# Performance work log

Hardware: AMD Instinct MI355X
Metric: run time of the kernel (lower is better)

The kernel has to match this reference:

```python
import jax, jax.numpy as jnp
import numpy as np

NUM_CLASSES = 2
THRESHOLD = 0.35
NEGPOS_RATIO = 7
VARIANCES = (0.1, 0.2)
B, P, O = 64, 16800, 64  # batch, num_priors, num_objs per image


def point_form(pr):
    # cxcywh -> xyxy
    return jnp.concatenate([pr[:, :2] - pr[:, 2:] / 2, pr[:, :2] + pr[:, 2:] / 2], axis=1)


def jaccard(a, b):
    # a: [A,4] xyxy, b: [Bx,4] xyxy -> IoU [A,Bx]
    lt = jnp.maximum(a[:, None, :2], b[None, :, :2])
    rb = jnp.minimum(a[:, None, 2:], b[None, :, 2:])
    wh = jnp.clip(rb - lt, 0.0)
    inter = wh[..., 0] * wh[..., 1]
    area_a = ((a[:, 2] - a[:, 0]) * (a[:, 3] - a[:, 1]))[:, None]
    area_b = ((b[:, 2] - b[:, 0]) * (b[:, 3] - b[:, 1]))[None, :]
    return inter / (area_a + area_b - inter)


def encode(matched, priors):
    # matched xyxy [P,4], priors cxcywh [P,4]
    g_cxcy = (matched[:, :2] + matched[:, 2:]) / 2 - priors[:, :2]
    g_cxcy = g_cxcy / (VARIANCES[0] * priors[:, 2:])
    g_wh = (matched[:, 2:] - matched[:, :2]) / priors[:, 2:]
    g_wh = jnp.log(g_wh) / VARIANCES[1]
    return jnp.concatenate([g_cxcy, g_wh], axis=1)


def encode_landm(matched, priors):
    # matched [P,10] -> [P,5,2]
    m = matched.reshape(-1, 5, 2)
    g = (m - priors[:, None, :2]) / (VARIANCES[0] * priors[:, None, 2:])
    return g.reshape(-1, 10)


def match_one(truths, labels, landms, priors):
    # truths [O,4], labels [O], landms [O,10]
    overlaps = jaccard(truths, point_form(priors))  # [O,P]
    best_prior_overlap = overlaps.max(axis=1)       # per-gt best IoU
    best_prior_idx = overlaps.argmax(axis=1)
    valid_gt = best_prior_overlap >= 0.2
    best_truth_overlap = overlaps.max(axis=0)       # per-prior best IoU
    best_truth_idx = overlaps.argmax(axis=0)
    # index_fill(2) only for valid gts (best_prior_idx_filter)
    bto = best_truth_overlap.at[best_prior_idx].set(
        jnp.where(valid_gt, 2.0, best_truth_overlap[best_prior_idx]))
    # ensure every gt keeps its best prior
    bti = best_truth_idx.at[best_prior_idx].set(jnp.arange(truths.shape[0]))
    matches = truths[bti]                  # [P,4]
    conf = labels[bti]                     # [P]
    conf = jnp.where(bto < THRESHOLD, 0.0, conf)
    loc = encode(matches, priors)
    landm = encode_landm(landms[bti], priors)
    return loc, conf, landm


def smooth_l1_sum(x, mask):
    ax = jnp.abs(x)
    v = jnp.where(ax < 1.0, 0.5 * ax * ax, ax - 0.5)
    return (v * mask).sum()


def setup_inputs() -> dict:
    key = jax.random.key(0)
    k1, k2, k3, k4, k5, k6, k7, k8 = jax.random.split(key, 8)
    loc_data = jax.random.normal(k1, (B, P, 4), jnp.float32)
    conf_data = jax.random.normal(k2, (B, P, NUM_CLASSES), jnp.float32)
    landm_data = jax.random.normal(k3, (B, P, 10), jnp.float32)
    # priors: cx,cy in (0,1), w,h in (0.02,0.22)
    cxy = jax.random.uniform(k4, (P, 2), jnp.float32)
    wh = jax.random.uniform(k5, (P, 2), jnp.float32) * 0.2 + 0.02
    priors = jnp.concatenate([cxy, wh], axis=1)
    # targets: valid corner boxes + landmarks + label in {1,-1}
    xy1 = jax.random.uniform(k6, (B, O, 2), jnp.float32) * 0.6
    bwh = jax.random.uniform(k7, (B, O, 2), jnp.float32) * 0.3 + 0.05
    boxes = jnp.concatenate([xy1, xy1 + bwh], axis=-1)
    lms = jax.random.uniform(k8, (B, O, 10), jnp.float32)
    lab = jnp.where(jax.random.uniform(jax.random.fold_in(key, 9), (B, O, 1)) < 0.3, -1.0, 1.0)
    targets = jnp.concatenate([boxes, lms, lab], axis=-1)
    return {"loc_data": loc_data, "conf_data": conf_data, "landm_data": landm_data,
            "priors": priors, "targets": targets}


def reference(loc_data, conf_data, landm_data, priors, targets):
    num = loc_data.shape[0]
    num_priors = priors.shape[0]
    truths = targets[:, :, :4]
    landms = targets[:, :, 4:14]
    labels = targets[:, :, -1]
    loc_t, conf_t, landm_t = jax.vmap(match_one, in_axes=(0, 0, 0, None))(
        truths, labels, landms, priors)  # [B,P,4], [B,P], [B,P,10]

    # landmark loss over conf_t > 0
    pos1 = conf_t > 0
    num_pos_landm = pos1.astype(jnp.int32).sum(axis=1, keepdims=True)
    N1 = jnp.maximum(num_pos_landm.sum().astype(jnp.float32), 1.0)
    loss_landm = smooth_l1_sum(landm_data - landm_t, pos1[..., None].astype(landm_data.dtype))

    # localization loss over conf_t != 0 ; conf_t[pos] = 1
    pos = conf_t != 0
    conf_t01 = jnp.where(pos, 1, 0)  # int {0,1}
    loss_l = smooth_l1_sum(loc_data - loc_t, pos[..., None].astype(loc_data.dtype))

    # hard negative mining on per-prior CE loss (global-max log_sum_exp, as in source)
    batch_conf = conf_data.reshape(-1, NUM_CLASSES)
    x_max = batch_conf.max()
    lse = jnp.log(jnp.exp(batch_conf - x_max).sum(axis=1, keepdims=True)) + x_max
    gathered = jnp.take_along_axis(batch_conf, conf_t01.reshape(-1, 1), axis=1)
    loss_c = (lse - gathered).reshape(num, -1)  # [B,P]; positives NOT zeroed (as in source)
    loss_idx = jnp.argsort(-loss_c, axis=1)
    idx_rank = jnp.argsort(loss_idx, axis=1)
    num_pos = pos.astype(jnp.int32).sum(axis=1, keepdims=True)  # [B,1]
    num_neg = jnp.minimum(NEGPOS_RATIO * num_pos, num_priors - 1)
    neg = idx_rank < num_neg  # [B,P]
    neg_pos = pos | neg

    # cross-entropy (sum) over selected pos+neg priors
    logp = jax.nn.log_softmax(conf_data, axis=-1)  # [B,P,C]
    ce = -jnp.take_along_axis(logp, conf_t01[..., None], axis=-1)[..., 0]
    loss_c_final = (ce * neg_pos.astype(ce.dtype)).sum()

    N = jnp.maximum(num_pos.sum().astype(jnp.float32), 1.0)
    return (loss_l / N, loss_c_final / N, loss_landm / N1)
```

## Files before the change

kernel.cpp:

```cpp
#include <hip/hip_runtime.h>
#include <math.h>

#define BN 64
#define PN 16800
#define ON 64
#define THRESH 0.35f
#define NEGPOS 7
#define GX 66
#define NBLK (BN * GX)
#define NBP 1024
#define NBTT (BN * GX)
#define NCELL 256
#define NBINS 4096
#define MAXM 4096
#define TAILT 104

struct GAcc {
  unsigned ticket;
  float sl, slm, sc;
  int np, np1;
  unsigned pad0, pad1;
};

__device__ __forceinline__ unsigned f2key(float f) {
  unsigned u = __float_as_uint(f);
  return (u & 0x80000000u) ? ~u : (u | 0x80000000u);
}
__device__ __forceinline__ float key2f(unsigned k) {
  unsigned u = (k & 0x80000000u) ? (k & 0x7FFFFFFFu) : ~k;
  return __uint_as_float(u);
}
__device__ __forceinline__ float sl1(float d) {
  float a = fabsf(d);
  return (a < 1.f) ? 0.5f * a * a : a - 0.5f;
}

__global__ void __launch_bounds__(1024) k_sort(const float* __restrict__ priors,
                                               float4* __restrict__ sbox,
                                               int* __restrict__ sorig,
                                               int* __restrict__ scell,
                                               int* __restrict__ inv,
                                               int* __restrict__ cellOff,
                                               unsigned* __restrict__ gmax,
                                               GAcc* __restrict__ gacc) {
  __shared__ unsigned cnt[NCELL];
  __shared__ unsigned cur[NCELL];
  __shared__ unsigned tmp[NCELL];
  int tid = threadIdx.x;
  if (tid < NCELL) cnt[tid] = 0;
  if (tid == 0) { gmax[0] = 0u; gmax[1] = 0u; }
  if (tid < 8) ((unsigned*)gacc)[tid] = 0;
  __syncthreads();
  float mw = 0.f, mh = 0.f;
  for (int p = tid; p < PN; p += 1024) {
    float4 pr = reinterpret_cast<const float4*>(priors)[p];
    int cx = (int)(pr.x * 16.f); cx = cx < 0 ? 0 : (cx > 15 ? 15 : cx);
    int cy = (int)(pr.y * 16.f); cy = cy < 0 ? 0 : (cy > 15 ? 15 : cy);
    atomicAdd(&cnt[cy * 16 + cx], 1u);
    mw = fmaxf(mw, pr.z * 0.5f);
    mh = fmaxf(mh, pr.w * 0.5f);
  }
#pragma unroll
  for (int off = 32; off; off >>= 1) {
    mw = fmaxf(mw, __shfl_xor(mw, off));
    mh = fmaxf(mh, __shfl_xor(mh, off));
  }
  if ((tid & 63) == 0) {
    atomicMax(&gmax[0], __float_as_uint(mw));
    atomicMax(&gmax[1], __float_as_uint(mh));
  }
  __syncthreads();
  if (tid < NCELL) tmp[tid] = cnt[tid];
  __syncthreads();
  for (int off = 1; off < NCELL; off <<= 1) {
    unsigned v = 0;
    if (tid < NCELL && tid >= off) v = tmp[tid - off];
    __syncthreads();
    if (tid < NCELL) tmp[tid] += v;
    __syncthreads();
  }
  if (tid < NCELL) {
    unsigned excl = tmp[tid] - cnt[tid];
    cur[tid] = excl;
    cellOff[tid] = (int)excl;
    if (tid == NCELL - 1) cellOff[NCELL] = (int)tmp[tid];
  }
  __syncthreads();
  for (int p = tid; p < PN; p += 1024) {
    float4 pr = reinterpret_cast<const float4*>(priors)[p];
    int cx = (int)(pr.x * 16.f); cx = cx < 0 ? 0 : (cx > 15 ? 15 : cx);
    int cy = (int)(pr.y * 16.f); cy = cy < 0 ? 0 : (cy > 15 ? 15 : cy);
    int cell = cy * 16 + cx;
    int s = (int)atomicAdd(&cur[cell], 1u);
    float px1 = pr.x - pr.z * 0.5f, py1 = pr.y - pr.w * 0.5f;
    float px2 = pr.x + pr.z * 0.5f, py2 = pr.y + pr.w * 0.5f;
    sbox[s] = make_float4(px1, py1, px2, py2);
    sorig[s] = p;
    scell[s] = cell;
    inv[p] = s;
  }
}

__global__ void k_masks(const float* __restrict__ targets,
                        const unsigned* __restrict__ gmax,
                        unsigned long long* __restrict__ tmask) {
  int b = blockIdx.x;
  int tid = threadIdx.x;
  __shared__ float4 tb[ON];
  if (tid < ON) {
    const float* tg = &targets[((long)b * ON + tid) * 15];
    tb[tid] = make_float4(tg[0], tg[1], tg[2], tg[3]);
  }
  __syncthreads();
  float MW = __uint_as_float(gmax[0]), MH = __uint_as_float(gmax[1]);
  int cx = tid & 15, cy = tid >> 4;
  float x0 = (float)(cx - 1) * 0.0625f - MW, x1 = (float)(cx + 2) * 0.0625f + MW;
  float y0 = (float)(cy - 1) * 0.0625f - MH, y1 = (float)(cy + 2) * 0.0625f + MH;
  unsigned long long m = 0ull;
  for (int t = 0; t < ON; t++) {
    float4 a = tb[t];
    if (x0 < a.z && x1 > a.x && y0 < a.w && y1 > a.y) m |= (1ull << t);
  }
  tmask[b * NCELL + tid] = m;
}

__global__ void k_pair(const float* __restrict__ targets,
                       const float4* __restrict__ sbox,
                       const int* __restrict__ sorig,
                       const int* __restrict__ scell,
                       const int* __restrict__ cellOff,
                       const unsigned* __restrict__ gmax,
                       const unsigned long long* __restrict__ tmask,
                       unsigned char* __restrict__ btpack,
                       unsigned long long* __restrict__ bpp) {
  int bid = blockIdx.x;
  int tid = threadIdx.x;

  if (bid < NBP) {
    int lane = tid & 63, wv = tid >> 6;
    int b = bid >> 4;
    int t = ((bid & 15) << 2) + wv;
    const float* tg = &targets[((long)b * ON + t) * 15];
    float ax1 = tg[0], ay1 = tg[1], ax2 = tg[2], ay2 = tg[3];
    float aa = (ax2 - ax1) * (ay2 - ay1);
    float MW = __uint_as_float(gmax[0]), MH = __uint_as_float(gmax[1]);
    int xlo = (int)floorf((ax1 - MW) * 16.f) - 1; xlo = xlo < 0 ? 0 : (xlo > 15 ? 15 : xlo);
    int xhi = (int)floorf((ax2 + MW) * 16.f) + 1; xhi = xhi < 0 ? 0 : (xhi > 15 ? 15 : xhi);
    int ylo = (int)floorf((ay1 - MH) * 16.f) - 1; ylo = ylo < 0 ? 0 : (ylo > 15 ? 15 : ylo);
    int yhi = (int)floorf((ay2 + MH) * 16.f) + 1; yhi = yhi < 0 ? 0 : (yhi > 15 ? 15 : yhi);
    float bi = 0.f, bu = 1.f; int bp = 0;
    for (int cy = ylo; cy <= yhi; cy++) {
      int s0 = cellOff[cy * 16 + xlo];
      int s1 = cellOff[cy * 16 + xhi + 1];
      for (int s = s0 + lane; s < s1; s += 64) {
        float4 pr = sbox[s];
        int op = sorig[s];
        float ab2 = (pr.z - pr.x) * (pr.w - pr.y);
        float lx = fmaxf(ax1, pr.x), ly = fmaxf(ay1, pr.y);
        float rx = fminf(ax2, pr.z), ry = fminf(ay2, pr.w);
        float w = fmaxf(rx - lx, 0.f), h = fmaxf(ry - ly, 0.f);
        float inter = w * h;
        float uni = aa + ab2 - inter;
        float A = inter * bu, C = bi * uni;
        if (A > C || (A == C && op < bp)) { bi = inter; bu = uni; bp = op; }
      }
    }
#pragma unroll
    for (int off = 1; off < 64; off <<= 1) {
      float oi = __shfl_xor(bi, off), ou = __shfl_xor(bu, off);
      int op = __shfl_xor(bp, off);
      float A = oi * bu, C = bi * ou;
      if (A > C || (A == C && op < bp)) { bi = oi; bu = ou; bp = op; }
    }
    if (lane == 0) {
      float q = bi / bu;
      bpp[(long)b * ON + t] = ((unsigned long long)f2key(q) << 32) | (unsigned)(~bp);
    }
  } else {
    int id2 = bid - NBP;
    int b = id2 / GX;
    int slab = id2 - b * GX;
    int s = slab * 256 + tid;
    bool valid = s < PN;
    int sc = valid ? s : PN - 1;
    __shared__ float4 tb[ON];
    __shared__ float ta[ON];
    if (tid < ON) {
      const float* tg = &targets[((long)b * ON + tid) * 15];
      float4 bx = make_float4(tg[0], tg[1], tg[2], tg[3]);
      tb[tid] = bx;
      ta[tid] = (bx.z - bx.x) * (bx.w - bx.y);
    }
    __syncthreads();
    float4 pr = sbox[sc];
    float ab2 = (pr.z - pr.x) * (pr.w - pr.y);
    unsigned long long um = valid ? tmask[b * NCELL + scell[sc]] : 0ull;
#pragma unroll
    for (int off = 1; off < 64; off <<= 1) um |= __shfl_xor(um, off);
    unsigned mlo = (unsigned)__builtin_amdgcn_readfirstlane((int)(unsigned)um);
    unsigned mhi = (unsigned)__builtin_amdgcn_readfirstlane((int)(unsigned)(um >> 32));
    unsigned long long m = ((unsigned long long)mhi << 32) | mlo;
    float bi = 0.f, bu = 1.f; int id = 0;
    while (m) {
      int t = __builtin_ctzll(m);
      m &= m - 1;
      float4 a = tb[t];
      float lx = fmaxf(a.x, pr.x), ly = fmaxf(a.y, pr.y);
      float rx = fminf(a.z, pr.z), ry = fminf(a.w, pr.w);
      float w = fmaxf(rx - lx, 0.f), h = fmaxf(ry - ly, 0.f);
      float inter = w * h;
      float uni = ta[t] + ab2 - inter;
      if (inter * bu > bi * uni) { bi = inter; bu = uni; id = t; }
    }
    if (valid) {
      float q = bi / bu;
      unsigned char posb = (q >= THRESH) ? 1 : 0;
      btpack[(long)b * PN + s] = (unsigned char)((id << 1) | posb);
    }
  }
}

__global__ void k_encode(const float* __restrict__ loc_data,
                         const float* __restrict__ conf_data,
                         const float* __restrict__ landm_data,
                         const float* __restrict__ priors,
                         const float* __restrict__ targets,
                         const unsigned char* __restrict__ btpack,
                         const int* __restrict__ inv,
                         const unsigned long long* __restrict__ bpp,
                         float* __restrict__ lossc, unsigned char* __restrict__ posf,
                         float* __restrict__ part_l, float* __restrict__ part_lm,
                         int* __restrict__ np_part, int* __restrict__ np1_part) {
  int b = blockIdx.y;
  int p = blockIdx.x * 256 + threadIdx.x;
  int bid = b * GX + blockIdx.x;
  __shared__ float4 tgs4[ON * 15 / 4];
  __shared__ int ovr[256];
  float* tgs = (float*)tgs4;
  if (threadIdx.x < ON * 15 / 4)
    tgs4[threadIdx.x] = reinterpret_cast<const float4*>(targets + (long)b * ON * 15)[threadIdx.x];
  ovr[threadIdx.x] = -1;
  __syncthreads();
  if (threadIdx.x < ON) {
    int t = threadIdx.x;
    unsigned long long best = bpp[(long)b * ON + t];
    float q = key2f((unsigned)(best >> 32));
    int qp = (int)(~(unsigned)best);
    int s0 = blockIdx.x * 256;
    if (qp >= s0 && qp < s0 + 256) {
      int valid = (q >= 0.2f) ? 1 : 0;
      atomicMax(&ovr[qp - s0], (t << 1) | valid);
    }
  }
  __syncthreads();

  float sum_l = 0.f, sum_lm = 0.f;
  int cp = 0, cp1 = 0;
  if (p < PN) {
    unsigned pk = btpack[(long)b * PN + inv[p]];
    int t = (int)(pk >> 1);
    bool pos = (pk & 1u) != 0;
    int o = ovr[threadIdx.x];
    if (o >= 0) { t = o >> 1; if (o & 1) pos = true; }
    const float* tg = &tgs[t * 15];
    float label = tg[14];
    bool pos1 = pos && (label > 0.f);
    float4 pr = reinterpret_cast<const float4*>(priors)[p];
    if (pos) {
      float rz = 1.0f / pr.z, rw = 1.0f / pr.w;
      float m0 = tg[0], m1 = tg[1], m2 = tg[2], m3 = tg[3];
      float g0 = ((m0 + m2) * 0.5f - pr.x) * rz * 10.f;
      float g1 = ((m1 + m3) * 0.5f - pr.y) * rw * 10.f;
      float g2 = __logf((m2 - m0) * rz) * 5.f;
      float g3 = __logf((m3 - m1) * rw) * 5.f;
      const float* ld = &loc_data[((long)b * PN + p) * 4];
      sum_l = sl1(ld[0] - g0) + sl1(ld[1] - g1) + sl1(ld[2] - g2) + sl1(ld[3] - g3);
      cp = 1;
      if (pos1) {
        const float* lm = &landm_data[((long)b * PN + p) * 10];
#pragma unroll
        for (int i = 0; i < 5; i++) {
          float gx = (tg[4 + 2 * i] - pr.x) * rz * 10.f;
          float gy = (tg[5 + 2 * i] - pr.y) * rw * 10.f;
          sum_lm += sl1(lm[2 * i] - gx) + sl1(lm[2 * i + 1] - gy);
        }
        cp1 = 1;
      }
    }
    float2 c2 = reinterpret_cast<const float2*>(conf_data)[(long)b * PN + p];
    float m = fmaxf(c2.x, c2.y);
    float lse = m + __logf(__expf(c2.x - m) + __expf(c2.y - m));
    lossc[b * PN + p] = lse - (pos ? c2.y : c2.x);
    posf[b * PN + p] = pos ? 1 : 0;
  }
  for (int off = 32; off; off >>= 1) {
    sum_l += __shfl_down(sum_l, off);
    sum_lm += __shfl_down(sum_lm, off);
    cp += __shfl_down(cp, off);
    cp1 += __shfl_down(cp1, off);
  }
  __shared__ float sl4[4], slm4[4];
  __shared__ int sp4[4], sp14[4];
  int w = threadIdx.x >> 6;
  if ((threadIdx.x & 63) == 0) { sl4[w] = sum_l; slm4[w] = sum_lm; sp4[w] = cp; sp14[w] = cp1; }
  __syncthreads();
  if (threadIdx.x == 0) {
    part_l[bid] = sl4[0] + sl4[1] + sl4[2] + sl4[3];
    part_lm[bid] = slm4[0] + slm4[1] + slm4[2] + slm4[3];
    np_part[bid] = sp4[0] + sp4[1] + sp4[2] + sp4[3];
    np1_part[bid] = sp14[0] + sp14[1] + sp14[2] + sp14[3];
  }
}

__global__ void __launch_bounds__(1024) k_select(const float* __restrict__ lossc,
                                                 const unsigned char* __restrict__ posf,
                                                 const int* __restrict__ np_part,
                                                 const int* __restrict__ np1_part,
                                                 const float* __restrict__ part_l,
                                                 const float* __restrict__ part_lm,
                                                 GAcc* __restrict__ gacc,
                                                 float* __restrict__ out) {
  int b = blockIdx.x;
  int tid = threadIdx.x;
  int lane = tid & 63;
  int wv = tid >> 6;
  __shared__ unsigned hist[NBINS];
  __shared__ unsigned wtot[16];
  __shared__ float resv[MAXM];
  __shared__ int residx[MAXM];
  __shared__ int s_np, s_B, s_kp;
  __shared__ unsigned s_mc;
  const float* row = &lossc[(long)b * PN];
  const unsigned char* prow = &posf[(long)b * PN];

  if (tid == 0) s_np = 0;
  for (int i = tid; i < NBINS; i += 1024) hist[i] = 0;
  __syncthreads();
  if (tid < GX) atomicAdd(&s_np, np_part[b * GX + tid]);

  const float4* rf4 = reinterpret_cast<const float4*>(row);
  const uint4* pw4 = reinterpret_cast<const uint4*>(prow);
  bool hasTail = tid < TAILT;
  float vm[16];
  float vt[4];
  {
    float4 L0 = rf4[tid * 4], L1 = rf4[tid * 4 + 1], L2 = rf4[tid * 4 + 2], L3 = rf4[tid * 4 + 3];
    vm[0] = L0.x; vm[1] = L0.y; vm[2] = L0.z; vm[3] = L0.w;
    vm[4] = L1.x; vm[5] = L1.y; vm[6] = L1.z; vm[7] = L1.w;
    vm[8] = L2.x; vm[9] = L2.y; vm[10] = L2.z; vm[11] = L2.w;
    vm[12] = L3.x; vm[13] = L3.y; vm[14] = L3.z; vm[15] = L3.w;
  }
  unsigned pmask = 0;
  {
    uint4 W = pw4[tid];
    unsigned w0 = W.x, w1 = W.y, w2 = W.z, w3 = W.w;
#pragma unroll
    for (int j = 0; j < 4; j++) {
      pmask |= ((w0 >> (8 * j)) & 1u) << j;
      pmask |= ((w1 >> (8 * j)) & 1u) << (4 + j);
      pmask |= ((w2 >> (8 * j)) & 1u) << (8 + j);
      pmask |= ((w3 >> (8 * j)) & 1u) << (12 + j);
    }
  }
  unsigned tmask = 0;
  if (hasTail) {
    float4 Lt = rf4[4096 + tid];
    vt[0] = Lt.x; vt[1] = Lt.y; vt[2] = Lt.z; vt[3] = Lt.w;
    unsigned Wt = reinterpret_cast<const unsigned*>(prow)[4096 + tid];
#pragma unroll
    for (int j = 0; j < 4; j++) tmask |= ((Wt >> (8 * j)) & 1u) << j;
  } else {
    vt[0] = vt[1] = vt[2] = vt[3] = -1.f;
  }
  int bm[16], bt4[4];
#pragma unroll
  for (int j = 0; j < 16; j++) {
    int q = (int)(vm[j] * 256.0f);
    bm[j] = q < 0 ? 0 : (q > NBINS - 1 ? NBINS - 1 : q);
  }
#pragma unroll
  for (int j = 0; j < 4; j++) {
    int q = (int)(vt[j] * 256.0f);
    bt4[j] = q < 0 ? 0 : (q > NBINS - 1 ? NBINS - 1 : q);
  }
  __syncthreads();
  int np = s_np;
  int k = NEGPOS * np;
  if (k > PN - 1) k = PN - 1;
  bool haveNeg = (k > 0);

  int B = NBINS, kp = 0, m = 0;
  bool allB = false, fallback = false;
  if (haveNeg) {
#pragma unroll
    for (int j = 0; j < 16; j++) atomicAdd(&hist[bm[j]], 1u);
    if (hasTail) {
#pragma unroll
      for (int j = 0; j < 4; j++) atomicAdd(&hist[bt4[j]], 1u);
    }
    __syncthreads();
    int t4 = tid * 4;
    unsigned h0 = hist[t4], h1 = hist[t4 + 1], h2 = hist[t4 + 2], h3 = hist[t4 + 3];
    unsigned th = h0 + h1 + h2 + h3;
    unsigned v = th;
#pragma unroll
    for (int off = 1; off < 64; off <<= 1) {
      unsigned tv = (unsigned)__shfl_down((int)v, off);
      if (lane + off < 64) v += tv;
    }
    if (lane == 0) wtot[wv] = v;
    __syncthreads();
    unsigned add = 0;
    for (int w2 = wv + 1; w2 < 16; w2++) add += wtot[w2];
    unsigned S_t = v + add;
    unsigned S_next = S_t - th;
    if (S_t >= (unsigned)k && S_next < (unsigned)k) {
      unsigned run = S_next; int Bl; unsigned kpl;
      if (run + h3 >= (unsigned)k) { Bl = t4 + 3; kpl = k - run; }
      else { run += h3;
        if (run + h2 >= (unsigned)k) { Bl = t4 + 2; kpl = k - run; }
        else { run += h2;
          if (run + h1 >= (unsigned)k) { Bl = t4 + 1; kpl = k - run; }
          else { run += h1; Bl = t4; kpl = k - run; } } }
      s_B = Bl; s_kp = (int)kpl;
    }
    __syncthreads();
    B = s_B; kp = s_kp; m = (int)hist[B];
    allB = (kp == m);
    fallback = (!allB && m > MAXM);
  }

  float acc = 0.f;
  if (haveNeg && !allB && !fallback) {
    if (tid == 0) s_mc = 0;
    __syncthreads();
#pragma unroll
    for (int j = 0; j < 16; j++) {
      if (bm[j] == B) {
        unsigned slot = atomicAdd(&s_mc, 1u);
        resv[slot] = vm[j];
        residx[slot] = (tid * 16 + j) | (((pmask >> j) & 1u) ? 0x40000000 : 0);
      }
    }
    if (hasTail) {
#pragma unroll
      for (int j = 0; j < 4; j++) {
        if (bt4[j] == B) {
          unsigned slot = atomicAdd(&s_mc, 1u);
          resv[slot] = vt[j];
          residx[slot] = (16384 + tid * 4 + j) | (((tmask >> j) & 1u) ? 0x40000000 : 0);
        }
      }
    }
    __syncthreads();
    for (int i = tid; i < m; i += 1024) {
      float vi = resv[i];
      int pk = residx[i];
      int ii = pk & 0x3FFFFFFF;
      bool posi = (pk & 0x40000000) != 0;
      int rank = 0;
      for (int j = 0; j < m; j++) {
        float vj = resv[j];
        int ij = residx[j] & 0x3FFFFFFF;
        rank += (vj > vi || (vj == vi && ij < ii)) ? 1 : 0;
      }
      if (rank < kp && !posi) acc += vi;
    }
  }

  unsigned T = 0, R = 0, C = 0;
  if (fallback) {
    __shared__ unsigned s_lo, s_hi, fcnt[16];
    if (tid == 0) { s_lo = 0u; s_hi = 0xFFFFFFFFu; }
    __syncthreads();
    for (int it = 0; it < 32; it++) {
      unsigned lo = s_lo, hi = s_hi;
      unsigned mid = lo + ((hi - lo) >> 1) + ((hi - lo) & 1u);
      unsigned c = 0;
#pragma unroll
      for (int j = 0; j < 16; j++) c += (f2key(vm[j]) >= mid) ? 1u : 0u;
      if (hasTail) {
#pragma unroll
        for (int j = 0; j < 4; j++) c += (f2key(vt[j]) >= mid) ? 1u : 0u;
      }
#pragma unroll
      for (int o = 32; o; o >>= 1) c += (unsigned)__shfl_down((int)c, o);
      if (lane == 0) fcnt[wv] = c;
      __syncthreads();
      if (tid == 0) {
        unsigned tot = 0;
        for (int i = 0; i < 16; i++) tot += fcnt[i];
        if (tot >= (unsigned)k) s_lo = mid; else s_hi = mid - 1;
      }
      __syncthreads();
      if (s_lo >= s_hi) break;
    }
    T = s_lo;
    unsigned cg = 0, ce = 0;
#pragma unroll
    for (int j = 0; j < 16; j++) {
      unsigned key = f2key(vm[j]);
      cg += (key > T) ? 1u : 0u;
      ce += (key == T) ? 1u : 0u;
    }
    if (hasTail) {
#pragma unroll
      for (int j = 0; j < 4; j++) {
        unsigned key = f2key(vt[j]);
        cg += (key > T) ? 1u : 0u;
        ce += (key == T) ? 1u : 0u;
      }
    }
#pragma unroll
    for (int o = 32; o; o >>= 1) {
      cg += (unsigned)__shfl_down((int)cg, o);
      ce += (unsigned)__shfl_down((int)ce, o);
    }
    if (lane == 0) { fcnt[wv] = cg; wtot[wv] = ce; }
    __syncthreads();
    if (tid == 0) {
      unsigned tg2 = 0, te = 0;
      for (int i = 0; i < 16; i++) { tg2 += fcnt[i]; te += wtot[i]; }
      fcnt[0] = tg2; wtot[0] = te;
    }
    __syncthreads();
    C = wtot[0];
    R = (unsigned)k - fcnt[0];
    if (C != R && tid < 64) {
      unsigned running = 0;
      for (int base2 = 0; base2 < PN; base2 += 64) {
        int p = base2 + tid;
        bool tie = false, pos = false;
        float v2 = 0.f;
        if (p < PN) { v2 = row[p]; tie = (f2key(v2) == T); pos = prow[p] != 0; }
        unsigned long long mm = __ballot(tie);
        if (tie) {
          unsigned rank = running + (unsigned)__popcll(mm & ((1ull << tid) - 1));
          if (rank < R && !pos) acc += v2;
        }
        running += (unsigned)__popcll(mm);
      }
    }
  }

  unsigned ptc = 0;
#pragma unroll
  for (int j = 0; j < 16; j++) {
    float v2 = vm[j];
    bool pos = (pmask >> j) & 1u;
    if (pos) acc += v2;
    else if (haveNeg) {
      if (!fallback) {
        if (bm[j] > B || (bm[j] == B && allB)) acc += v2;
      } else {
        if (f2key(v2) > T) acc += v2;
      }
    }
    if (fallback && pos && f2key(v2) == T) ptc++;
  }
  if (hasTail) {
#pragma unroll
    for (int j = 0; j < 4; j++) {
      float v2 = vt[j];
      bool pos = (tmask >> j) & 1u;
      if (pos) acc += v2;
      else if (haveNeg) {
        if (!fallback) {
          if (bt4[j] > B || (bt4[j] == B && allB)) acc += v2;
        } else {
          if (f2key(v2) > T) acc += v2;
        }
      }
      if (fallback && pos && f2key(v2) == T) ptc++;
    }
  }
  for (int o = 32; o; o >>= 1) {
    acc += __shfl_down(acc, o);
    ptc += __shfl_down(ptc, o);
  }
  __shared__ float wsum[16];
  __shared__ unsigned wpt[16];
  if (lane == 0) { wsum[wv] = acc; wpt[wv] = ptc; }
  __syncthreads();

  __shared__ float s_rsl, s_rslm;
  __shared__ int s_rnp1;
  if (tid == 0) { s_rsl = 0.f; s_rslm = 0.f; s_rnp1 = 0; }
  __syncthreads();
  if (tid < GX) {
    atomicAdd(&s_rsl, part_l[b * GX + tid]);
    atomicAdd(&s_rslm, part_lm[b * GX + tid]);
    atomicAdd(&s_rnp1, np1_part[b * GX + tid]);
  }
  __syncthreads();

  if (tid == 0) {
    float tot = 0.f; unsigned pt = 0;
    for (int i = 0; i < 16; i++) { tot += wsum[i]; pt += wpt[i]; }
    if (fallback && C == R) tot += (float)(C - pt) * key2f(T);
    atomicAdd(&gacc->sc, tot);
    atomicAdd(&gacc->sl, s_rsl);
    atomicAdd(&gacc->slm, s_rslm);
    atomicAdd(&gacc->np, np);
    atomicAdd(&gacc->np1, s_rnp1);
  }
  __threadfence();
  __shared__ int lastF;
  if (tid == 0) lastF = (atomicAdd(&gacc->ticket, 1u) == (unsigned)(BN - 1)) ? 1 : 0;
  __syncthreads();
  if (lastF && tid == 0) {
    __threadfence();
    float sl = atomicAdd(&gacc->sl, 0.f);
    float slm = atomicAdd(&gacc->slm, 0.f);
    float sc = atomicAdd(&gacc->sc, 0.f);
    int tnp = atomicAdd(&gacc->np, 0);
    int tnp1 = atomicAdd(&gacc->np1, 0);
    float N = fmaxf((float)tnp, 1.f);
    float N1 = fmaxf((float)tnp1, 1.f);
    out[0] = sl / N;
    out[1] = sc / N;
    out[2] = slm / N1;
  }
}

extern "C" void kernel_launch(void* const* d_in, const int* in_sizes, int n_in,
                              void* d_out, int out_size, void* d_ws, size_t ws_size,
                              hipStream_t stream) {
  const float* loc_data = (const float*)d_in[0];
  const float* conf_data = (const float*)d_in[1];
  const float* landm_data = (const float*)d_in[2];
  const float* priors = (const float*)d_in[3];
  const float* targets = (const float*)d_in[4];
  float* out = (float*)d_out;

  char* ws = (char*)d_ws;
  size_t off = 0;
  float* lossc = (float*)(ws + off); off += (size_t)BN * PN * 4;
  unsigned char* btpack = (unsigned char*)(ws + off); off += (size_t)BN * PN;
  unsigned char* posf = (unsigned char*)(ws + off); off += (size_t)BN * PN;
  off = (off + 15) & ~(size_t)15;
  unsigned long long* bpp = (unsigned long long*)(ws + off); off += (size_t)BN * ON * 8;
  float* part_l = (float*)(ws + off); off += NBLK * 4;
  float* part_lm = (float*)(ws + off); off += NBLK * 4;
  int* np_part = (int*)(ws + off); off += NBLK * 4;
  int* np1_part = (int*)(ws + off); off += NBLK * 4;
  float4* sbox = (float4*)(ws + off); off += (size_t)PN * 16;
  int* sorig = (int*)(ws + off); off += (size_t)PN * 4;
  int* scell = (int*)(ws + off); off += (size_t)PN * 4;
  int* inv = (int*)(ws + off); off += (size_t)PN * 4;
  int* cellOff = (int*)(ws + off); off += 260 * 4;
  unsigned* gmax = (unsigned*)(ws + off); off += 16;
  unsigned long long* tmask = (unsigned long long*)(ws + off); off += (size_t)BN * NCELL * 8;
  GAcc* gacc = (GAcc*)(ws + off); off += sizeof(GAcc);

  k_sort<<<1, 1024, 0, stream>>>(priors, sbox, sorig, scell, inv, cellOff, gmax, gacc);
  k_masks<<<BN, 256, 0, stream>>>(targets, gmax, tmask);
  k_pair<<<NBP + NBTT, 256, 0, stream>>>(targets, sbox, sorig, scell, cellOff, gmax,
                                         tmask, btpack, bpp);
  dim3 gbp(GX, BN);
  k_encode<<<gbp, 256, 0, stream>>>(loc_data, conf_data, landm_data, priors, targets,
                                    btpack, inv, bpp, lossc, posf,
                                    part_l, part_lm, np_part, np1_part);
  k_select<<<BN, 1024, 0, stream>>>(lossc, posf, np_part, np1_part, part_l, part_lm,
                                    gacc, out);
}
```

Measured before the change: 226.5 us.

## Split single-block prior sort into multi-block count and scatter kernels

Replaces the single 1024-thread prior binning and sort kernel with a 66-block counting kernel that uses global atomics, followed by a scatter kernel. In the scatter kernel every block recomputes the prefix scan and reserves its slots per cell with atomics. The tmask construction is folded into the scatter kernel as extra blocks, and a memset zeroes the global counters. The IoU candidate loop in k_pair is also unrolled by two so that two gt boxes are handled per iteration. The cost is one extra launch plus a memset and redundant scans in each block, and the order of priors within a cell stays nondeterministic.

```diff
diff --git a/kernel.cpp b/kernel.cpp
--- a/kernel.cpp
+++ b/kernel.cpp
@@ -11,6 +11,7 @@
 #define NBP 1024
 #define NBTT (BN * GX)
 #define NCELL 256
+#define NCB 66
 #define NBINS 4096
 #define MAXM 4096
 #define TAILT 104
@@ -35,93 +36,114 @@
   return (a < 1.f) ? 0.5f * a * a : a - 0.5f;
 }
 
-__global__ void __launch_bounds__(1024) k_sort(const float* __restrict__ priors,
-                                               float4* __restrict__ sbox,
-                                               int* __restrict__ sorig,
-                                               int* __restrict__ scell,
-                                               int* __restrict__ inv,
-                                               int* __restrict__ cellOff,
-                                               unsigned* __restrict__ gmax,
-                                               GAcc* __restrict__ gacc) {
-  __shared__ unsigned cnt[NCELL];
-  __shared__ unsigned cur[NCELL];
-  __shared__ unsigned tmp[NCELL];
+__global__ void k_count(const float* __restrict__ priors,
+                        unsigned char* __restrict__ pcell,
+                        unsigned* __restrict__ gcnt,
+                        unsigned* __restrict__ gmax) {
+  __shared__ unsigned lcnt[NCELL];
   int tid = threadIdx.x;
-  if (tid < NCELL) cnt[tid] = 0;
-  if (tid == 0) { gmax[0] = 0u; gmax[1] = 0u; }
-  if (tid < 8) ((unsigned*)gacc)[tid] = 0;
-  __syncthreads();
+  lcnt[tid] = 0;
+  __syncthreads();
+  int p = blockIdx.x * 256 + tid;
   float mw = 0.f, mh = 0.f;
-  for (int p = tid; p < PN; p += 1024) {
-    float4 pr = reinterpret_cast<const float4*>(priors)[p];
-    int cx = (int)(pr.x * 16.f); cx = cx < 0 ? 0 : (cx > 15 ? 15 : cx);
-    int cy = (int)(pr.y * 16.f); cy = cy < 0 ? 0 : (cy > 15 ? 15 : cy);
-    atomicAdd(&cnt[cy * 16 + cx], 1u);
-    mw = fmaxf(mw, pr.z * 0.5f);
-    mh = fmaxf(mh, pr.w * 0.5f);
-  }
-#pragma unroll
-  for (int off = 32; off; off >>= 1) {
-    mw = fmaxf(mw, __shfl_xor(mw, off));
-    mh = fmaxf(mh, __shfl_xor(mh, off));
-  }
-  if ((tid & 63) == 0) {
-    atomicMax(&gmax[0], __float_as_uint(mw));
-    atomicMax(&gmax[1], __float_as_uint(mh));
-  }
-  __syncthreads();
-  if (tid < NCELL) tmp[tid] = cnt[tid];
-  __syncthreads();
-  for (int off = 1; off < NCELL; off <<= 1) {
-    unsigned v = 0;
-    if (tid < NCELL && tid >= off) v = tmp[tid - off];
-    __syncthreads();
-    if (tid < NCELL) tmp[tid] += v;
-    __syncthreads();
-  }
-  if (tid < NCELL) {
-    unsigned excl = tmp[tid] - cnt[tid];
-    cur[tid] = excl;
-    cellOff[tid] = (int)excl;
-    if (tid == NCELL - 1) cellOff[NCELL] = (int)tmp[tid];
-  }
-  __syncthreads();
-  for (int p = tid; p < PN; p += 1024) {
+  if (p < PN) {
     float4 pr = reinterpret_cast<const float4*>(priors)[p];
     int cx = (int)(pr.x * 16.f); cx = cx < 0 ? 0 : (cx > 15 ? 15 : cx);
     int cy = (int)(pr.y * 16.f); cy = cy < 0 ? 0 : (cy > 15 ? 15 : cy);
     int cell = cy * 16 + cx;
-    int s = (int)atomicAdd(&cur[cell], 1u);
-    float px1 = pr.x - pr.z * 0.5f, py1 = pr.y - pr.w * 0.5f;
-    float px2 = pr.x + pr.z * 0.5f, py2 = pr.y + pr.w * 0.5f;
-    sbox[s] = make_float4(px1, py1, px2, py2);
-    sorig[s] = p;
-    scell[s] = cell;
-    inv[p] = s;
-  }
-}
-
-__global__ void k_masks(const float* __restrict__ targets,
-                        const unsigned* __restrict__ gmax,
-                        unsigned long long* __restrict__ tmask) {
-  int b = blockIdx.x;
+    pcell[p] = (unsigned char)cell;
+    atomicAdd(&lcnt[cell], 1u);
+    mw = pr.z * 0.5f;
+    mh = pr.w * 0.5f;
+  }
+#pragma unroll
+  for (int off = 32; off; off >>= 1) {
+    mw = fmaxf(mw, __shfl_xor(mw, off));
+    mh = fmaxf(mh, __shfl_xor(mh, off));
+  }
+  if ((tid & 63) == 0) {
+    atomicMax(&gmax[0], __float_as_uint(mw));
+    atomicMax(&gmax[1], __float_as_uint(mh));
+  }
+  __syncthreads();
+  unsigned c = lcnt[tid];
+  if (c) atomicAdd(&gcnt[tid], c);
+}
+
+__global__ void k_scatter(const float* __restrict__ priors,
+                          const float* __restrict__ targets,
+                          const unsigned char* __restrict__ pcell,
+                          const unsigned* __restrict__ gcnt,
+                          unsigned* __restrict__ gcur,
+                          const unsigned* __restrict__ gmax,
+                          float4* __restrict__ sbox,
+                          int* __restrict__ sorig,
+                          int* __restrict__ scell,
+                          int* __restrict__ inv,
+                          int* __restrict__ cellOff,
+                          unsigned long long* __restrict__ tmask) {
+  int bid = blockIdx.x;
   int tid = threadIdx.x;
-  __shared__ float4 tb[ON];
-  if (tid < ON) {
-    const float* tg = &targets[((long)b * ON + tid) * 15];
-    tb[tid] = make_float4(tg[0], tg[1], tg[2], tg[3]);
-  }
-  __syncthreads();
-  float MW = __uint_as_float(gmax[0]), MH = __uint_as_float(gmax[1]);
-  int cx = tid & 15, cy = tid >> 4;
-  float x0 = (float)(cx - 1) * 0.0625f - MW, x1 = (float)(cx + 2) * 0.0625f + MW;
-  float y0 = (float)(cy - 1) * 0.0625f - MH, y1 = (float)(cy + 2) * 0.0625f + MH;
-  unsigned long long m = 0ull;
-  for (int t = 0; t < ON; t++) {
-    float4 a = tb[t];
-    if (x0 < a.z && x1 > a.x && y0 < a.w && y1 > a.y) m |= (1ull << t);
-  }
-  tmask[b * NCELL + tid] = m;
+  if (bid < NCB) {
+    __shared__ unsigned tmp[NCELL];
+    __shared__ unsigned excl[NCELL];
+    __shared__ unsigned lcnt[NCELL];
+    __shared__ unsigned lbase[NCELL];
+    unsigned c = gcnt[tid];
+    tmp[tid] = c;
+    lcnt[tid] = 0;
+    __syncthreads();
+    for (int off = 1; off < NCELL; off <<= 1) {
+      unsigned v = (tid >= off) ? tmp[tid - off] : 0u;
+      __syncthreads();
+      tmp[tid] += v;
+      __syncthreads();
+    }
+    excl[tid] = tmp[tid] - c;
+    if (bid == 0) {
+      cellOff[tid] = (int)(tmp[tid] - c);
+      if (tid == 0) cellOff[NCELL] = PN;
+    }
+    __syncthreads();
+    int p = bid * 256 + tid;
+    bool valid = p < PN;
+    int cell = 0; unsigned lrank = 0;
+    if (valid) {
+      cell = pcell[p];
+      lrank = atomicAdd(&lcnt[cell], 1u);
+    }
+    __syncthreads();
+    if (lcnt[tid]) lbase[tid] = atomicAdd(&gcur[tid], lcnt[tid]);
+    __syncthreads();
+    if (valid) {
+      int slot = (int)(excl[cell] + lbase[cell] + lrank);
+      float4 pr = reinterpret_cast<const float4*>(priors)[p];
+      float px1 = pr.x - pr.z * 0.5f, py1 = pr.y - pr.w * 0.5f;
+      float px2 = pr.x + pr.z * 0.5f, py2 = pr.y + pr.w * 0.5f;
+      sbox[slot] = make_float4(px1, py1, px2, py2);
+      sorig[slot] = p;
+      scell[slot] = cell;
+      inv[p] = slot;
+    }
+  } else {
+    int b = bid - NCB;
+    __shared__ float4 tb[ON];
+    if (tid < ON) {
+      const float* tg = &targets[((long)b * ON + tid) * 15];
+      tb[tid] = make_float4(tg[0], tg[1], tg[2], tg[3]);
+    }
+    __syncthreads();
+    float MW = __uint_as_float(gmax[0]), MH = __uint_as_float(gmax[1]);
+    int cx = tid & 15, cy = tid >> 4;
+    float x0 = (float)(cx - 1) * 0.0625f - MW, x1 = (float)(cx + 2) * 0.0625f + MW;
+    float y0 = (float)(cy - 1) * 0.0625f - MH, y1 = (float)(cy + 2) * 0.0625f + MH;
+    unsigned long long m = 0ull;
+    for (int t = 0; t < ON; t++) {
+      float4 a = tb[t];
+      if (x0 < a.z && x1 > a.x && y0 < a.w && y1 > a.y) m |= (1ull << t);
+    }
+    tmask[b * NCELL + tid] = m;
+  }
 }
 
 __global__ void k_pair(const float* __restrict__ targets,
@@ -202,15 +224,29 @@
     unsigned long long m = ((unsigned long long)mhi << 32) | mlo;
     float bi = 0.f, bu = 1.f; int id = 0;
     while (m) {
-      int t = __builtin_ctzll(m);
-      m &= m - 1;
-      float4 a = tb[t];
-      float lx = fmaxf(a.x, pr.x), ly = fmaxf(a.y, pr.y);
-      float rx = fminf(a.z, pr.z), ry = fminf(a.w, pr.w);
-      float w = fmaxf(rx - lx, 0.f), h = fmaxf(ry - ly, 0.f);
-      float inter = w * h;
-      float uni = ta[t] + ab2 - inter;
-      if (inter * bu > bi * uni) { bi = inter; bu = uni; id = t; }
+      int t0 = __builtin_ctzll(m); m &= m - 1;
+      float4 a0 = tb[t0]; float aa0 = ta[t0];
+      if (m) {
+        int t1 = __builtin_ctzll(m); m &= m - 1;
+        float4 a1 = tb[t1]; float aa1 = ta[t1];
+        float lx0 = fmaxf(a0.x, pr.x), ly0 = fmaxf(a0.y, pr.y);
+        float rx0 = fminf(a0.z, pr.z), ry0 = fminf(a0.w, pr.w);
+        float w0 = fmaxf(rx0 - lx0, 0.f), h0 = fmaxf(ry0 - ly0, 0.f);
+        float in0 = w0 * h0, un0 = aa0 + ab2 - in0;
+        float lx1 = fmaxf(a1.x, pr.x), ly1 = fmaxf(a1.y, pr.y);
+        float rx1 = fminf(a1.z, pr.z), ry1 = fminf(a1.w, pr.w);
+        float w1 = fmaxf(rx1 - lx1, 0.f), h1 = fmaxf(ry1 - ly1, 0.f);
+        float in1 = w1 * h1, un1 = aa1 + ab2 - in1;
+        if (in0 * bu > bi * un0) { bi = in0; bu = un0; id = t0; }
+        if (in1 * bu > bi * un1) { bi = in1; bu = un1; id = t1; }
+      } else {
+        float lx = fmaxf(a0.x, pr.x), ly = fmaxf(a0.y, pr.y);
+        float rx = fminf(a0.z, pr.z), ry = fminf(a0.w, pr.w);
+        float w = fmaxf(rx - lx, 0.f), h = fmaxf(ry - ly, 0.f);
+        float inter = w * h;
+        float uni = aa0 + ab2 - inter;
+        if (inter * bu > bi * uni) { bi = inter; bu = uni; id = t0; }
+      }
     }
     if (valid) {
       float q = bi / bu;
@@ -648,13 +684,23 @@
   int* sorig = (int*)(ws + off); off += (size_t)PN * 4;
   int* scell = (int*)(ws + off); off += (size_t)PN * 4;
   int* inv = (int*)(ws + off); off += (size_t)PN * 4;
+  unsigned char* pcell = (unsigned char*)(ws + off); off += (size_t)PN;
+  off = (off + 15) & ~(size_t)15;
   int* cellOff = (int*)(ws + off); off += 260 * 4;
-  unsigned* gmax = (unsigned*)(ws + off); off += 16;
   unsigned long long* tmask = (unsigned long long*)(ws + off); off += (size_t)BN * NCELL * 8;
-  GAcc* gacc = (GAcc*)(ws + off); off += sizeof(GAcc);
-
-  k_sort<<<1, 1024, 0, stream>>>(priors, sbox, sorig, scell, inv, cellOff, gmax, gacc);
-  k_masks<<<BN, 256, 0, stream>>>(targets, gmax, tmask);
+  off = (off + 15) & ~(size_t)15;
+  unsigned* zreg = (unsigned*)(ws + off);
+  unsigned* gcnt = zreg;
+  unsigned* gcur = zreg + 256;
+  unsigned* gmax = zreg + 512;
+  GAcc* gacc = (GAcc*)(zreg + 516);
+  size_t zbytes = (256 + 256 + 4) * 4 + sizeof(GAcc);
+  off += zbytes;
+
+  hipMemsetAsync(zreg, 0, zbytes, stream);
+  k_count<<<NCB, 256, 0, stream>>>(priors, pcell, gcnt, gmax);
+  k_scatter<<<NCB + BN, 256, 0, stream>>>(priors, targets, pcell, gcnt, gcur, gmax,
+                                          sbox, sorig, scell, inv, cellOff, tmask);
   k_pair<<<NBP + NBTT, 256, 0, stream>>>(targets, sbox, sorig, scell, cellOff, gmax,
                                          tmask, btpack, bpp);
   dim3 gbp(GX, BN);
```

After: 200.5 us. -11.5%, faster.
